# Kernel optimization log

Hardware: AMD Instinct MI355X
Metric: run time of the kernel (lower is better)

The kernel has to match this reference:

```python
import jax, jax.numpy as jnp
import numpy as np

N_NODES = 100000
N_EDGES = 800000
N_IN = 256
N_H = 128


def setup_inputs() -> dict:
    key = jax.random.key(0)
    ks = jax.random.split(key, 8)
    x_1 = jax.random.normal(ks[0], (1, N_NODES, N_IN), dtype=jnp.float32)
    x_2 = jax.random.normal(ks[1], (1, N_NODES, N_IN), dtype=jnp.float32)
    edge_index = jax.random.randint(ks[2], (2, N_EDGES), 0, N_NODES, dtype=jnp.int32)
    edge_weight = jax.random.uniform(ks[3], (N_EDGES,), dtype=jnp.float32)
    # xavier-uniform-ish init for fc weight (stored as [in, out])
    lim = float(np.sqrt(6.0 / (N_IN + N_H)))
    W_gcn = jax.random.uniform(ks[4], (N_IN, N_H), minval=-lim, maxval=lim, dtype=jnp.float32)
    gcn_bias = jnp.zeros((N_H,), dtype=jnp.float32)
    prelu_a = jnp.full((1,), 0.25, dtype=jnp.float32)  # PReLU default slope
    lim2 = float(np.sqrt(1.0 / N_H))
    lin_W = jax.random.uniform(ks[5], (N_H, N_H), minval=-lim2, maxval=lim2, dtype=jnp.float32)
    lin_b = jax.random.uniform(ks[6], (N_H,), minval=-lim2, maxval=lim2, dtype=jnp.float32)
    return {
        "x_1": x_1, "x_2": x_2, "edge_index": edge_index, "edge_weight": edge_weight,
        "W_gcn": W_gcn, "gcn_bias": gcn_bias, "prelu_a": prelu_a,
        "lin_W": lin_W, "lin_b": lin_b,
    }


def _prelu(x, a):
    return jnp.where(x >= 0, x, a * x)


def _gcn(feat, edge_index, edge_weight, W, b, a, n_nodes):
    # feat: [1, N, n_in] -> h: [N, n_h]
    h = jnp.squeeze(feat, 0) @ W
    row, col = edge_index[0], edge_index[1]
    # spmm: out[i] = sum_{e: row_e = i} w_e * h[col_e]
    msg = edge_weight[:, None] * h[col]            # [E, n_h]
    agg = jax.ops.segment_sum(msg, row, num_segments=n_nodes)  # [N, n_h]
    return _prelu(agg + b, a)                      # [N, n_h]


def reference(x_1, x_2, edge_index, edge_weight, W_gcn, gcn_bias, prelu_a, lin_W, lin_b):
    n = x_1.shape[1]
    h_1 = _gcn(x_1, edge_index, edge_weight, W_gcn, gcn_bias, prelu_a, n)
    h_2 = _gcn(x_2, edge_index, edge_weight, W_gcn, gcn_bias, prelu_a, n)
    z_1 = (h_1 @ lin_W + lin_b).sum(1)   # [N]
    z_2 = (h_2 @ lin_W + lin_b).sum(1)   # [N]
    return jnp.concatenate((z_1, z_2), 0)  # [2N]
```

## Files before the change

### kernel.cpp

```cpp
#include <hip/hip_runtime.h>

#define N_NODES 100000
#define N_EDGES 800000
#define N_IN    256
#define N_H     128
#define M_TOT   (2 * N_NODES)

typedef __bf16 bfx8 __attribute__((ext_vector_type(8)));
typedef unsigned short u16x8 __attribute__((ext_vector_type(8)));
typedef float fx4 __attribute__((ext_vector_type(4)));

__device__ inline unsigned short f2bf(float f) {
    union { float f; unsigned u; } v; v.f = f;
    return (unsigned short)((v.u + 0x7FFF + ((v.u >> 16) & 1)) >> 16);
}
__device__ inline float bf2f(unsigned short s) {
    union { unsigned u; float f; } v; v.u = ((unsigned)s) << 16;
    return v.f;
}

__device__ inline void async16(const void* g, void* l) {
    __builtin_amdgcn_global_load_lds((const __attribute__((address_space(1))) void*)g,
                                     (__attribute__((address_space(3))) void*)l, 16, 0, 0);
}

#define NTB1  6250
#define NSB   3125
#define NGB   12500

__global__ __launch_bounds__(256, 4) void gemm_scatter_kernel(
        const float* __restrict__ x1, const float* __restrict__ x2,
        const unsigned short* __restrict__ wT,
        unsigned short* __restrict__ hb,
        const int* __restrict__ ei, const float* __restrict__ ew,
        int* __restrict__ cursor, int2* __restrict__ edata) {
    const int t = threadIdx.x;
    if (blockIdx.x < NSB) {
        int e = blockIdx.x * 256 + t;
        int row = ei[e];
        int pos = atomicAdd(cursor + row, 1);
        edata[pos] = make_int2(ei[N_EDGES + e] << 8, __float_as_int(ew[e]));
        return;
    }
    __shared__ __align__(16) float Abuf[16][256];
    const int T = blockIdx.x - NSB;
    const int wv = t >> 6, ln = t & 63;
    const int quad = ln >> 4, l16 = ln & 15, sw = l16 & 7;
    const int br = T >= NTB1;
    const float* xs = br ? x2 : x1;
    const int node0 = (T - br * NTB1) * 16;
    const float* base = xs + (size_t)node0 * N_IN;

#pragma unroll
    for (int i = 0; i < 4; ++i) {
        int r = wv * 4 + i;
        async16(base + (size_t)r * N_IN + ((ln ^ (r & 7)) << 2), &Abuf[r][0]);
    }

    bfx8 Bf[2][8];
#pragma unroll
    for (int c2 = 0; c2 < 2; ++c2)
#pragma unroll
        for (int kc = 0; kc < 8; ++kc)
            Bf[c2][kc] = *(const bfx8*)(wT +
                (size_t)(wv * 32 + c2 * 16 + l16) * N_IN + kc * 32 + quad * 8);

    __syncthreads();

    fx4 acc0 = {0.f, 0.f, 0.f, 0.f}, acc1 = {0.f, 0.f, 0.f, 0.f};
    const float* rowp = &Abuf[l16][0];
#pragma unroll
    for (int kc = 0; kc < 8; ++kc) {
        int s0 = kc * 8 + quad * 2;
        fx4 lo = *(const fx4*)(rowp + (((s0    ) ^ sw) << 2));
        fx4 hi = *(const fx4*)(rowp + (((s0 + 1) ^ sw) << 2));
        bfx8 af;
        af[0] = (__bf16)lo[0]; af[1] = (__bf16)lo[1];
        af[2] = (__bf16)lo[2]; af[3] = (__bf16)lo[3];
        af[4] = (__bf16)hi[0]; af[5] = (__bf16)hi[1];
        af[6] = (__bf16)hi[2]; af[7] = (__bf16)hi[3];
        acc0 = __builtin_amdgcn_mfma_f32_16x16x32_bf16(af, Bf[0][kc], acc0, 0, 0, 0);
        acc1 = __builtin_amdgcn_mfma_f32_16x16x32_bf16(af, Bf[1][kc], acc1, 0, 0, 0);
    }
    unsigned short* hp = hb + (size_t)node0 * 256 + br * 128 + wv * 32 + l16;
#pragma unroll
    for (int r = 0; r < 4; ++r) {
        size_t off = (size_t)(quad * 4 + r) * 256;
        hp[off]      = __builtin_bit_cast(unsigned short, (__bf16)acc0[r]);
        hp[off + 16] = __builtin_bit_cast(unsigned short, (__bf16)acc1[r]);
    }
}

#define HIST_BLKS 3125
__global__ __launch_bounds__(256) void prep_kernel(const int* __restrict__ ei,
                                                   int* __restrict__ deg,
                                                   const float* __restrict__ W,
                                                   unsigned short* __restrict__ wT,
                                                   const float* __restrict__ linW,
                                                   const float* __restrict__ linb,
                                                   float* __restrict__ wsum) {
    const int t = threadIdx.x;
    if (blockIdx.x < HIST_BLKS) {
        int e = blockIdx.x * 256 + t;
        if (e < N_EDGES) atomicAdd(deg + ei[e], 1);
    } else if (blockIdx.x < HIST_BLKS + 32) {
        int kb = (blockIdx.x - HIST_BLKS) * 8;
#pragma unroll
        for (int p = 0; p < 4; ++p) {
            int idx = p * 256 + t;
            int k = kb + (idx >> 7), n = idx & 127;
            wT[(size_t)n * N_IN + k] = f2bf(W[(size_t)k * N_H + n]);
        }
    } else {
        __shared__ float part[N_H];
        if (t < N_H) part[t] = 0.f;
        __syncthreads();
        const int wvp = t >> 6, lnp = t & 63;
        for (int ii = 0; ii < 64; ++ii) {
            float v = linW[ii * 256 + t];
#pragma unroll
            for (int o = 32; o; o >>= 1) v += __shfl_down(v, o, 64);
            if (lnp == 0) atomicAdd(&part[2 * ii + (wvp >> 1)], v);
        }
        __syncthreads();
        if (t < N_H) wsum[t] = part[t];
        if (wvp == 2) {
            float v = linb[lnp] + linb[lnp + 64];
#pragma unroll
            for (int o = 32; o; o >>= 1) v += __shfl_down(v, o, 64);
            if (lnp == 0) wsum[N_H] = v;
        }
    }
}

__global__ __launch_bounds__(256) void scan1_kernel(const int* __restrict__ deg,
                                                    int* __restrict__ part,
                                                    int* __restrict__ bsum) {
    __shared__ int s[256];
    int g = blockIdx.x * 256 + threadIdx.x;
    int v = (g < N_NODES) ? deg[g] : 0;
    s[threadIdx.x] = v;
    __syncthreads();
#pragma unroll
    for (int off = 1; off < 256; off <<= 1) {
        int t = (threadIdx.x >= off) ? s[threadIdx.x - off] : 0;
        __syncthreads();
        s[threadIdx.x] += t;
        __syncthreads();
    }
    if (g < N_NODES) part[g] = s[threadIdx.x] - v;
    if (threadIdx.x == 255) bsum[blockIdx.x] = s[255];
}

#define NBLK_SCAN 391
__global__ void scan2_kernel(int* __restrict__ bsum) {
    __shared__ int s[512];
    int v = (threadIdx.x < NBLK_SCAN) ? bsum[threadIdx.x] : 0;
    s[threadIdx.x] = v;
    __syncthreads();
#pragma unroll
    for (int off = 1; off < 512; off <<= 1) {
        int t = (threadIdx.x >= off) ? s[threadIdx.x - off] : 0;
        __syncthreads();
        s[threadIdx.x] += t;
        __syncthreads();
    }
    if (threadIdx.x < NBLK_SCAN) bsum[threadIdx.x] = s[threadIdx.x] - v;
}

__global__ __launch_bounds__(256) void scan3_kernel(const int* __restrict__ part,
                                                    const int* __restrict__ bsum,
                                                    int* __restrict__ off,
                                                    int* __restrict__ cursor) {
    int g = blockIdx.x * 256 + threadIdx.x;
    if (g < N_NODES) {
        int o = part[g] + bsum[blockIdx.x];
        off[g] = o;
        cursor[g] = o;
    }
    if (g == 0) off[N_NODES] = N_EDGES;
}

__global__ __launch_bounds__(256) void gcn_seg_kernel(const int* __restrict__ off,
                                                      const int2* __restrict__ edata,
                                                      const unsigned short* __restrict__ hb,
                                                      const float* __restrict__ gcn_bias,
                                                      const float* __restrict__ prelu_a,
                                                      const float* __restrict__ wsum,
                                                      float* __restrict__ zout) {
    const int wave = threadIdx.x >> 6, lane = threadIdx.x & 63;
    const int node = blockIdx.x * 4 + wave;
    const int s = __builtin_amdgcn_readfirstlane(off[node]);
    const int e = __builtin_amdgcn_readfirstlane(off[node + 1]);
    const int l2 = lane * 2;
    float a0 = 0.f, a1 = 0.f;
    float b0 = 0.f, b1 = 0.f;
    int i = s;
    for (; i + 3 < e; i += 4) {
        int2 E0 = edata[i], E1 = edata[i + 1];
        int2 E2 = edata[i + 2], E3 = edata[i + 3];
        float w0 = __int_as_float(E0.y), w1 = __int_as_float(E1.y);
        float w2 = __int_as_float(E2.y), w3 = __int_as_float(E3.y);
        ushort2 p10 = *(const ushort2*)(hb + E0.x + l2);
        ushort2 p20 = *(const ushort2*)(hb + E0.x + 128 + l2);
        ushort2 p11 = *(const ushort2*)(hb + E1.x + l2);
        ushort2 p21 = *(const ushort2*)(hb + E1.x + 128 + l2);
        ushort2 p12 = *(const ushort2*)(hb + E2.x + l2);
        ushort2 p22 = *(const ushort2*)(hb + E2.x + 128 + l2);
        ushort2 p13 = *(const ushort2*)(hb + E3.x + l2);
        ushort2 p23 = *(const ushort2*)(hb + E3.x + 128 + l2);
        a0 += w0 * bf2f(p10.x) + w1 * bf2f(p11.x) + w2 * bf2f(p12.x) + w3 * bf2f(p13.x);
        a1 += w0 * bf2f(p10.y) + w1 * bf2f(p11.y) + w2 * bf2f(p12.y) + w3 * bf2f(p13.y);
        b0 += w0 * bf2f(p20.x) + w1 * bf2f(p21.x) + w2 * bf2f(p22.x) + w3 * bf2f(p23.x);
        b1 += w0 * bf2f(p20.y) + w1 * bf2f(p21.y) + w2 * bf2f(p22.y) + w3 * bf2f(p23.y);
    }
    for (; i < e; ++i) {
        int2 E0 = edata[i];
        float w0 = __int_as_float(E0.y);
        ushort2 p10 = *(const ushort2*)(hb + E0.x + l2);
        ushort2 p20 = *(const ushort2*)(hb + E0.x + 128 + l2);
        a0 += w0 * bf2f(p10.x);
        a1 += w0 * bf2f(p10.y);
        b0 += w0 * bf2f(p20.x);
        b1 += w0 * bf2f(p20.y);
    }
    const float alpha = prelu_a[0];
    const float g0 = gcn_bias[l2], g1 = gcn_bias[l2 + 1];
    const float q0 = wsum[l2],     q1 = wsum[l2 + 1];
    float v0 = a0 + g0, v1 = a1 + g1;
    float u0 = b0 + g0, u1 = b1 + g1;
    v0 = (v0 >= 0.f) ? v0 : alpha * v0;
    v1 = (v1 >= 0.f) ? v1 : alpha * v1;
    u0 = (u0 >= 0.f) ? u0 : alpha * u0;
    u1 = (u1 >= 0.f) ? u1 : alpha * u1;
    float s1 = v0 * q0 + v1 * q1;
    float s2 = u0 * q0 + u1 * q1;
#pragma unroll
    for (int o = 32; o; o >>= 1) {
        s1 += __shfl_down(s1, o, 64);
        s2 += __shfl_down(s2, o, 64);
    }
    if (lane == 0) {
        zout[node]           = s1 + wsum[128];
        zout[node + N_NODES] = s2 + wsum[128];
    }
}

extern "C" void kernel_launch(void* const* d_in, const int* in_sizes, int n_in,
                              void* d_out, int out_size, void* d_ws, size_t ws_size,
                              hipStream_t stream) {
    const float* x1 = (const float*)d_in[0];
    const float* x2 = (const float*)d_in[1];
    const int*   ei = (const int*)d_in[2];
    const float* ew = (const float*)d_in[3];
    const float* Wg = (const float*)d_in[4];
    const float* gb = (const float*)d_in[5];
    const float* pa = (const float*)d_in[6];
    const float* lW = (const float*)d_in[7];
    const float* lb = (const float*)d_in[8];
    float* zout = (float*)d_out;

    unsigned short* hb   = (unsigned short*)d_ws;
    int2*  edata  = (int2*)(hb + (size_t)M_TOT * N_H);
    unsigned short* wT   = (unsigned short*)(edata + N_EDGES);
    int*   deg    = (int*)(wT + N_IN * N_H);
    int*   part   = deg + 100096;
    int*   off    = part + 100096;
    int*   cursor = off + 100096;
    int*   bsum   = cursor + 100096;
    float* wsum   = (float*)(bsum + 512);

    hipMemsetAsync(deg, 0, (size_t)N_NODES * sizeof(int), stream);
    prep_kernel<<<HIST_BLKS + 33, 256, 0, stream>>>(ei, deg, Wg, wT, lW, lb, wsum);
    scan1_kernel<<<NBLK_SCAN, 256, 0, stream>>>(deg, part, bsum);
    scan2_kernel<<<1, 512, 0, stream>>>(bsum);
    scan3_kernel<<<NBLK_SCAN, 256, 0, stream>>>(part, bsum, off, cursor);
    gemm_scatter_kernel<<<NSB + NGB, 256, 0, stream>>>(x1, x2, wT, hb,
                                                       ei, ew, cursor, edata);
    gcn_seg_kernel<<<N_NODES / 4, 256, 0, stream>>>(off, edata, hb, gb, pa, wsum, zout);
}
```

Baseline: 457.7 us.

## Fuse degree histogram into GEMM launch and load X directly to registers

The degree histogram blocks move from the prep kernel into the GEMM kernel, so the histogram atomics overlap the feature GEMM. The edge scatter becomes its own kernel after the scan. The GEMM now loads its A operand straight from global memory into registers instead of staging it in LDS with async loads and a barrier, and the launch-bounds occupancy hint drops from 4 to 3. The segment-sum loop is unrolled by 2 instead of 4, which lowers register use but leaves fewer gathers in flight.

```diff
diff --git a/kernel.cpp b/kernel.cpp
--- a/kernel.cpp
+++ b/kernel.cpp
@@ -19,44 +19,35 @@
     return v.f;
 }
 
-__device__ inline void async16(const void* g, void* l) {
-    __builtin_amdgcn_global_load_lds((const __attribute__((address_space(1))) void*)g,
-                                     (__attribute__((address_space(3))) void*)l, 16, 0, 0);
-}
-
-#define NTB1  6250
-#define NSB   3125
-#define NGB   12500
-
-__global__ __launch_bounds__(256, 4) void gemm_scatter_kernel(
+#define NTB1      6250
+#define NGB       12500
+#define HIST_BLKS 3125
+
+__global__ __launch_bounds__(256, 3) void gemm_hist_kernel(
         const float* __restrict__ x1, const float* __restrict__ x2,
         const unsigned short* __restrict__ wT,
         unsigned short* __restrict__ hb,
-        const int* __restrict__ ei, const float* __restrict__ ew,
-        int* __restrict__ cursor, int2* __restrict__ edata) {
+        const int* __restrict__ ei, int* __restrict__ deg) {
     const int t = threadIdx.x;
-    if (blockIdx.x < NSB) {
-        int e = blockIdx.x * 256 + t;
-        int row = ei[e];
-        int pos = atomicAdd(cursor + row, 1);
-        edata[pos] = make_int2(ei[N_EDGES + e] << 8, __float_as_int(ew[e]));
+    if (blockIdx.x >= NGB) {
+        int e = (blockIdx.x - NGB) * 256 + t;
+        atomicAdd(deg + ei[e], 1);
         return;
     }
-    __shared__ __align__(16) float Abuf[16][256];
-    const int T = blockIdx.x - NSB;
+    const int T = blockIdx.x;
     const int wv = t >> 6, ln = t & 63;
-    const int quad = ln >> 4, l16 = ln & 15, sw = l16 & 7;
+    const int quad = ln >> 4, l16 = ln & 15;
     const int br = T >= NTB1;
     const float* xs = br ? x2 : x1;
     const int node0 = (T - br * NTB1) * 16;
-    const float* base = xs + (size_t)node0 * N_IN;
-
-#pragma unroll
-    for (int i = 0; i < 4; ++i) {
-        int r = wv * 4 + i;
-        async16(base + (size_t)r * N_IN + ((ln ^ (r & 7)) << 2), &Abuf[r][0]);
-    }
-
+    const float* xrow = xs + (size_t)node0 * N_IN + (size_t)l16 * N_IN;
+
+    float4 xa[8], xb[8];
+#pragma unroll
+    for (int kc = 0; kc < 8; ++kc) {
+        xa[kc] = *(const float4*)(xrow + kc * 32 + quad * 8);
+        xb[kc] = *(const float4*)(xrow + kc * 32 + quad * 8 + 4);
+    }
     bfx8 Bf[2][8];
 #pragma unroll
     for (int c2 = 0; c2 < 2; ++c2)
@@ -65,20 +56,14 @@
             Bf[c2][kc] = *(const bfx8*)(wT +
                 (size_t)(wv * 32 + c2 * 16 + l16) * N_IN + kc * 32 + quad * 8);
 
-    __syncthreads();
-
     fx4 acc0 = {0.f, 0.f, 0.f, 0.f}, acc1 = {0.f, 0.f, 0.f, 0.f};
-    const float* rowp = &Abuf[l16][0];
 #pragma unroll
     for (int kc = 0; kc < 8; ++kc) {
-        int s0 = kc * 8 + quad * 2;
-        fx4 lo = *(const fx4*)(rowp + (((s0    ) ^ sw) << 2));
-        fx4 hi = *(const fx4*)(rowp + (((s0 + 1) ^ sw) << 2));
         bfx8 af;
-        af[0] = (__bf16)lo[0]; af[1] = (__bf16)lo[1];
-        af[2] = (__bf16)lo[2]; af[3] = (__bf16)lo[3];
-        af[4] = (__bf16)hi[0]; af[5] = (__bf16)hi[1];
-        af[6] = (__bf16)hi[2]; af[7] = (__bf16)hi[3];
+        af[0] = (__bf16)xa[kc].x; af[1] = (__bf16)xa[kc].y;
+        af[2] = (__bf16)xa[kc].z; af[3] = (__bf16)xa[kc].w;
+        af[4] = (__bf16)xb[kc].x; af[5] = (__bf16)xb[kc].y;
+        af[6] = (__bf16)xb[kc].z; af[7] = (__bf16)xb[kc].w;
         acc0 = __builtin_amdgcn_mfma_f32_16x16x32_bf16(af, Bf[0][kc], acc0, 0, 0, 0);
         acc1 = __builtin_amdgcn_mfma_f32_16x16x32_bf16(af, Bf[1][kc], acc1, 0, 0, 0);
     }
@@ -91,20 +76,24 @@
     }
 }
 
-#define HIST_BLKS 3125
-__global__ __launch_bounds__(256) void prep_kernel(const int* __restrict__ ei,
-                                                   int* __restrict__ deg,
-                                                   const float* __restrict__ W,
+#define NSB  3125
+__global__ __launch_bounds__(256) void scatter_kernel(
+        const int* __restrict__ ei, const float* __restrict__ ew,
+        int* __restrict__ cursor, int2* __restrict__ edata) {
+    int e = blockIdx.x * 256 + threadIdx.x;
+    int row = ei[e];
+    int pos = atomicAdd(cursor + row, 1);
+    edata[pos] = make_int2(ei[N_EDGES + e] << 8, __float_as_int(ew[e]));
+}
+
+__global__ __launch_bounds__(256) void prep_kernel(const float* __restrict__ W,
                                                    unsigned short* __restrict__ wT,
                                                    const float* __restrict__ linW,
                                                    const float* __restrict__ linb,
                                                    float* __restrict__ wsum) {
     const int t = threadIdx.x;
-    if (blockIdx.x < HIST_BLKS) {
-        int e = blockIdx.x * 256 + t;
-        if (e < N_EDGES) atomicAdd(deg + ei[e], 1);
-    } else if (blockIdx.x < HIST_BLKS + 32) {
-        int kb = (blockIdx.x - HIST_BLKS) * 8;
+    if (blockIdx.x < 32) {
+        int kb = blockIdx.x * 8;
 #pragma unroll
         for (int p = 0; p < 4; ++p) {
             int idx = p * 256 + t;
@@ -196,25 +185,19 @@
     float a0 = 0.f, a1 = 0.f;
     float b0 = 0.f, b1 = 0.f;
     int i = s;
-    for (; i + 3 < e; i += 4) {
+    for (; i + 1 < e; i += 2) {
         int2 E0 = edata[i], E1 = edata[i + 1];
-        int2 E2 = edata[i + 2], E3 = edata[i + 3];
         float w0 = __int_as_float(E0.y), w1 = __int_as_float(E1.y);
-        float w2 = __int_as_float(E2.y), w3 = __int_as_float(E3.y);
         ushort2 p10 = *(const ushort2*)(hb + E0.x + l2);
         ushort2 p20 = *(const ushort2*)(hb + E0.x + 128 + l2);
         ushort2 p11 = *(const ushort2*)(hb + E1.x + l2);
         ushort2 p21 = *(const ushort2*)(hb + E1.x + 128 + l2);
-        ushort2 p12 = *(const ushort2*)(hb + E2.x + l2);
-        ushort2 p22 = *(const ushort2*)(hb + E2.x + 128 + l2);
-        ushort2 p13 = *(const ushort2*)(hb + E3.x + l2);
-        ushort2 p23 = *(const ushort2*)(hb + E3.x + 128 + l2);
-        a0 += w0 * bf2f(p10.x) + w1 * bf2f(p11.x) + w2 * bf2f(p12.x) + w3 * bf2f(p13.x);
-        a1 += w0 * bf2f(p10.y) + w1 * bf2f(p11.y) + w2 * bf2f(p12.y) + w3 * bf2f(p13.y);
-        b0 += w0 * bf2f(p20.x) + w1 * bf2f(p21.x) + w2 * bf2f(p22.x) + w3 * bf2f(p23.x);
-        b1 += w0 * bf2f(p20.y) + w1 * bf2f(p21.y) + w2 * bf2f(p22.y) + w3 * bf2f(p23.y);
-    }
-    for (; i < e; ++i) {
+        a0 += w0 * bf2f(p10.x) + w1 * bf2f(p11.x);
+        a1 += w0 * bf2f(p10.y) + w1 * bf2f(p11.y);
+        b0 += w0 * bf2f(p20.x) + w1 * bf2f(p21.x);
+        b1 += w0 * bf2f(p20.y) + w1 * bf2f(p21.y);
+    }
+    if (i < e) {
         int2 E0 = edata[i];
         float w0 = __int_as_float(E0.y);
         ushort2 p10 = *(const ushort2*)(hb + E0.x + l2);
@@ -271,11 +254,11 @@
     float* wsum   = (float*)(bsum + 512);
 
     hipMemsetAsync(deg, 0, (size_t)N_NODES * sizeof(int), stream);
-    prep_kernel<<<HIST_BLKS + 33, 256, 0, stream>>>(ei, deg, Wg, wT, lW, lb, wsum);
+    prep_kernel<<<33, 256, 0, stream>>>(Wg, wT, lW, lb, wsum);
+    gemm_hist_kernel<<<NGB + HIST_BLKS, 256, 0, stream>>>(x1, x2, wT, hb, ei, deg);
     scan1_kernel<<<NBLK_SCAN, 256, 0, stream>>>(deg, part, bsum);
     scan2_kernel<<<1, 512, 0, stream>>>(bsum);
     scan3_kernel<<<NBLK_SCAN, 256, 0, stream>>>(part, bsum, off, cursor);
-    gemm_scatter_kernel<<<NSB + NGB, 256, 0, stream>>>(x1, x2, wT, hb,
-                                                       ei, ew, cursor, edata);
+    scatter_kernel<<<NSB, 256, 0, stream>>>(ei, ew, cursor, edata);
     gcn_seg_kernel<<<N_NODES / 4, 256, 0, stream>>>(off, edata, hb, gb, pa, wsum, zout);
 }
```

Measured after the change: 528.9 us. 1.16x slower.
